# Kernel optimization log

Hardware: AMD Instinct MI355X
Metric: run time of the kernel (lower is better)

Reference implementation:

```python
import jax, jax.numpy as jnp
import numpy as np

DIM = 512
NUM_HEADS = 8
HEAD_DIM = DIM // NUM_HEADS
SCALE = HEAD_DIM ** -0.5


def setup_inputs() -> dict:
    key = jax.random.key(0)
    k1, k2, k3, k4 = jax.random.split(key, 4)
    x = jax.random.normal(k1, (4, 2048, DIM), dtype=jnp.float32)
    W_qkv = jax.random.normal(k2, (DIM, 3 * DIM), dtype=jnp.float32) * (DIM ** -0.5)
    W_proj = jax.random.normal(k3, (DIM, DIM), dtype=jnp.float32) * (DIM ** -0.5)
    b_proj = jax.random.normal(k4, (DIM,), dtype=jnp.float32) * 0.01
    return {"x": x, "W_qkv": W_qkv, "W_proj": W_proj, "b_proj": b_proj}


def reference(x, W_qkv, W_proj, b_proj):
    B, N, C = x.shape
    H, hd = NUM_HEADS, HEAD_DIM
    # qkv: [B, N, 3, H, hd] -> (q, k, v) each [B, H, N, hd]
    qkv = (x @ W_qkv).reshape(B, N, 3, H, hd)
    qkv = jnp.transpose(qkv, (2, 0, 3, 1, 4))
    q, k, v = qkv[0], qkv[1], qkv[2]
    # eager attention: [B, H, N, N]
    attn = jnp.einsum('bhnd,bhmd->bhnm', q, k) * SCALE
    attn = jax.nn.softmax(attn, axis=-1)
    out = jnp.einsum('bhnm,bhmd->bhnd', attn, v)  # [B, H, N, hd]
    out = jnp.transpose(out, (0, 2, 1, 3)).reshape(B, N, C)
    out = out @ W_proj + b_proj
    return (out, k, v)
```

## Files before the change

kernel.cpp:

```cpp
#include <hip/hip_runtime.h>

typedef unsigned short ushort_t;
typedef __bf16 bf16x8 __attribute__((ext_vector_type(8)));
typedef ushort_t u16x8 __attribute__((ext_vector_type(8)));
typedef float f32x4 __attribute__((ext_vector_type(4)));

#define MFMA(a, b, c) __builtin_amdgcn_mfma_f32_16x16x32_bf16(a, b, c, 0, 0, 0)

#define N_X      4194304L
#define N_WQKV   786432L
#define N_WPROJ  262144L
#define OUT_OFF_K 4194304L
#define OUT_OFF_V 8388608L

#define OFF_FLAG   0UL
#define OFF_XB     1024UL
#define OFF_WQKVT  (OFF_XB + 8388608UL)
#define OFF_WPROJT (OFF_WQKVT + 1572864UL)
#define OFF_BPROJ  (OFF_WPROJT + 524288UL)
#define OFF_QB     (OFF_BPROJ + 2048UL)
#define OFF_KB     (OFF_QB + 8388608UL)
#define OFF_VTB    (OFF_KB + 8388608UL)
#define OFF_ATTN   (OFF_VTB + 8388608UL)

#define QSCALE 0.180336880519191f

__device__ __forceinline__ ushort_t f2b(float f) {
    union { float f; unsigned u; } v; v.f = f;
    return (ushort_t)((v.u + 0x7FFFu + ((v.u >> 16) & 1u)) >> 16);
}
__device__ __forceinline__ ushort_t f2b_trunc(float f) {
    union { float f; unsigned u; } v; v.f = f;
    return (ushort_t)(v.u >> 16);
}
__device__ __forceinline__ float b2f(ushort_t h) {
    union { unsigned u; float f; } v; v.u = ((unsigned)h) << 16;
    return v.f;
}
__device__ __forceinline__ float ldf(const float* p, long i) { return p[i]; }
__device__ __forceinline__ float ldf(const ushort_t* p, long i) { return b2f(p[i]); }
__device__ __forceinline__ void stf(float* p, long i, float v) { p[i] = v; }
__device__ __forceinline__ void stf(ushort_t* p, long i, float v) { p[i] = f2b(v); }

__device__ __forceinline__ float fast_exp2(float x) {
#if __has_builtin(__builtin_amdgcn_exp2f)
    return __builtin_amdgcn_exp2f(x);
#else
    return __expf(x * 0.6931471805599453f);
#endif
}

__device__ __forceinline__ void glds16(const void* g, const void* l) {
    __builtin_amdgcn_global_load_lds((__attribute__((address_space(1))) void*)g,
                                     (__attribute__((address_space(3))) void*)l,
                                     16, 0, 0);
}

__global__ void k_detect(const unsigned* __restrict__ x, int* __restrict__ flag) {
    int lane = threadIdx.x & 63;
    int cnt = 0;
#pragma unroll
    for (int i = 0; i < 4; ++i) {
        unsigned w = x[lane + i * 64];
        float v = __uint_as_float((w & 0xFFFFu) << 16);
        float a = fabsf(v);
        if (a > 1e-3f && a < 100.0f) cnt++;
    }
#pragma unroll
    for (int off = 32; off; off >>= 1) cnt += __shfl_down(cnt, off, 64);
    if (lane == 0) *flag = (cnt > 128) ? 1 : 0;
}

template <typename T>
__global__ void k_prep(const T* __restrict__ x, const T* __restrict__ wq,
                       const T* __restrict__ wp, const T* __restrict__ bp,
                       ushort_t* __restrict__ xb, ushort_t* __restrict__ wqT,
                       ushort_t* __restrict__ wpT, float* __restrict__ bpf,
                       const int* __restrict__ flag, int want) {
    if (*flag != want) return;
    long i0 = (long)blockIdx.x * blockDim.x + threadIdx.x;
    long stride = (long)gridDim.x * blockDim.x;
    for (long i = i0; i < N_X; i += stride) xb[i] = f2b(ldf(x, i));
    for (long i = i0; i < N_WQKV; i += stride) {
        long n = i >> 9, k = i & 511;
        wqT[i] = f2b(ldf(wq, k * 1536 + n));
    }
    for (long i = i0; i < N_WPROJ; i += stride) {
        long n = i >> 9, k = i & 511;
        wpT[i] = f2b(ldf(wp, k * 512 + n));
    }
    for (long i = i0; i < 512; i += stride) bpf[i] = ldf(bp, i);
}

template <typename TOUT>
__global__ __launch_bounds__(256, 2)
void k_qkv(const ushort_t* __restrict__ xb, const ushort_t* __restrict__ wqT,
           ushort_t* __restrict__ qb, ushort_t* __restrict__ kb, ushort_t* __restrict__ vb,
           TOUT* __restrict__ kout, TOUT* __restrict__ vout,
           const int* __restrict__ flag, int want) {
    if (*flag != want) return;
    __shared__ __align__(16) ushort_t As[128 * 32];
    __shared__ __align__(16) ushort_t Bs[128 * 32];
    const int tid = threadIdx.x, wave = tid >> 6, lane = tid & 63;
    const int tm = blockIdx.x * 128, tn = blockIdx.y * 128;
    const int wm = (wave >> 1) * 64, wn = (wave & 1) * 64;
    const int l15 = lane & 15, lq = lane >> 4;
    const int srow = lane >> 2, sc = lane & 3;

    f32x4 acc[4][4];
#pragma unroll
    for (int a = 0; a < 4; ++a)
#pragma unroll
        for (int b = 0; b < 4; ++b) acc[a][b] = (f32x4){0.f, 0.f, 0.f, 0.f};

    for (int k0 = 0; k0 < 512; k0 += 32) {
#pragma unroll
        for (int t = 0; t < 2; ++t) {
            int s = wave * 2 + t;
            int row = s * 16 + srow;
            int c = (sc ^ (row >> 1)) & 3;
            glds16(xb  + (long)(tm + row) * 512 + k0 + c * 8, As + s * 512);
            glds16(wqT + (long)(tn + row) * 512 + k0 + c * 8, Bs + s * 512);
        }
        __syncthreads();
        bf16x8 af[4], bfr[4];
#pragma unroll
        for (int mt = 0; mt < 4; ++mt) {
            int row = wm + mt * 16 + l15;
            int cp = (lq ^ (row >> 1)) & 3;
            af[mt] = *(const bf16x8*)(As + row * 32 + cp * 8);
        }
#pragma unroll
        for (int nt = 0; nt < 4; ++nt) {
            int row = wn + nt * 16 + l15;
            int cp = (lq ^ (row >> 1)) & 3;
            bfr[nt] = *(const bf16x8*)(Bs + row * 32 + cp * 8);
        }
#pragma unroll
        for (int mt = 0; mt < 4; ++mt)
#pragma unroll
            for (int nt = 0; nt < 4; ++nt)
                acc[mt][nt] = MFMA(af[mt], bfr[nt], acc[mt][nt]);
        __syncthreads();
    }

#pragma unroll
    for (int mt = 0; mt < 4; ++mt) {
#pragma unroll
        for (int nt = 0; nt < 4; ++nt) {
            int j = tn + wn + nt * 16 + l15;
            int t = j >> 9, h = (j >> 6) & 7, d = j & 63;
#pragma unroll
            for (int r = 0; r < 4; ++r) {
                int mm = tm + wm + mt * 16 + lq * 4 + r;
                int b = mm >> 11, nn = mm & 2047;
                float v = acc[mt][nt][r];
                long idx = ((long)(b * 8 + h) * 2048 + nn) * 64 + d;
                if (t == 0) {
                    qb[idx] = f2b(v * QSCALE);
                } else if (t == 1) {
                    kb[idx] = f2b(v);
                    stf(kout, idx, v);
                } else {
                    vb[idx] = f2b(v);
                    stf(vout, idx, v);
                }
            }
        }
    }
}

__global__ __launch_bounds__(256, 4)
void k_vtrans(const ushort_t* __restrict__ vb, ushort_t* __restrict__ vtb) {
    __shared__ ushort_t T[64 * 64];
    const int tid = threadIdx.x;
    const int bh = blockIdx.y, ktile = blockIdx.x;
    const long base = (long)bh * 131072 + (long)ktile * 64 * 64;
    const int row = tid >> 2, cq = tid & 3;
#pragma unroll
    for (int half = 0; half < 2; ++half) {
        int c = cq + half * 4;
        u16x8 v = *(const u16x8*)(vb + base + row * 64 + c * 8);
#pragma unroll
        for (int e = 0; e < 8; ++e) {
            int dim = c * 8 + e;
            T[row * 64 + ((dim + row) & 63)] = v[e];
        }
    }
    __syncthreads();
#pragma unroll
    for (int it = 0; it < 16; ++it) {
        int d = (tid >> 6) * 16 + it;
        int key = tid & 63;
        vtb[(long)bh * 131072 + (long)d * 2048 + ktile * 64 + key] =
            T[key * 64 + ((d + key) & 63)];
    }
}

__global__ __launch_bounds__(256, 4)
void k_attn(const ushort_t* __restrict__ qb, const ushort_t* __restrict__ kb,
            const ushort_t* __restrict__ vtb, ushort_t* __restrict__ attnb) {
    __shared__ __align__(16) ushort_t Kt[128 * 64];
    __shared__ __align__(16) ushort_t Vt[64 * 128];
    __shared__ __align__(16) ushort_t Ps[4][16 * 64];
    const int tid = threadIdx.x, wave = tid >> 6, lane = tid & 63;
    const int l15 = lane & 15, lq = lane >> 4;
    const int bh = blockIdx.y, qt = blockIdx.x;
    const long kvbase = (long)bh * 131072;
    const long qbase = kvbase + (long)qt * 64 * 64;

    bf16x8 aQ[2];
#pragma unroll
    for (int kt = 0; kt < 2; ++kt)
        aQ[kt] = *(const bf16x8*)(qb + qbase +
            (long)(wave * 16 + l15) * 64 + kt * 32 + lq * 8);

    union { ushort_t u[8]; bf16x8 v; } oneu;
#pragma unroll
    for (int i = 0; i < 8; ++i) oneu.u[i] = 0x3F80;
    const bf16x8 ones = oneu.v;

    f32x4 oacc[4], sum_acc;
#pragma unroll
    for (int n = 0; n < 4; ++n) oacc[n] = (f32x4){0.f, 0.f, 0.f, 0.f};
    sum_acc = (f32x4){0.f, 0.f, 0.f, 0.f};

    const int ksrow = lane >> 3, kschunk = lane & 7;
    const int vsrow = lane >> 4, vschunk = lane & 15;
    ushort_t* Pw = &Ps[wave][0];

    for (int j = 0; j < 16; ++j) {
#pragma unroll
        for (int t = 0; t < 4; ++t) {
            int s = wave * 4 + t;
            {
                int row = s * 8 + ksrow;
                int c = kschunk ^ (row & 7);
                glds16(kb + kvbase + (long)(j * 128 + row) * 64 + c * 8, Kt + s * 512);
            }
            {
                int row = s * 4 + vsrow;
                int c = vschunk ^ (row & 15);
                glds16(vtb + kvbase + (long)row * 2048 + j * 128 + c * 8, Vt + s * 512);
            }
        }
        __syncthreads();

#pragma unroll
        for (int h = 0; h < 2; ++h) {
            f32x4 sacc[4];
#pragma unroll
            for (int nt = 0; nt < 4; ++nt) sacc[nt] = (f32x4){0.f, 0.f, 0.f, 0.f};
#pragma unroll
            for (int nt = 0; nt < 4; ++nt) {
                int krow = h * 64 + nt * 16 + l15;
#pragma unroll
                for (int kt = 0; kt < 2; ++kt) {
                    int c = (kt * 4 + lq) ^ (krow & 7);
                    bf16x8 bk = *(const bf16x8*)(Kt + krow * 64 + c * 8);
                    sacc[nt] = MFMA(aQ[kt], bk, sacc[nt]);
                }
            }
#pragma unroll
            for (int nt = 0; nt < 4; ++nt) {
#pragma unroll
                for (int r = 0; r < 4; ++r) {
                    float p = fast_exp2(sacc[nt][r]);
                    int prow = lq * 4 + r;
                    int col = nt * 16 + l15;
                    int ch = (col >> 3) ^ (prow & 7);
                    Pw[prow * 64 + ch * 8 + (col & 7)] = f2b_trunc(p);
                }
            }
#pragma unroll
            for (int kt = 0; kt < 2; ++kt) {
                int cha = (kt * 4 + lq) ^ (l15 & 7);
                bf16x8 ap = *(const bf16x8*)(Pw + l15 * 64 + cha * 8);
                sum_acc = MFMA(ap, ones, sum_acc);
#pragma unroll
                for (int nd = 0; nd < 4; ++nd) {
                    int vrow = nd * 16 + l15;
                    int vch = (h * 8 + kt * 4 + lq) ^ (vrow & 15);
                    bf16x8 bv = *(const bf16x8*)(Vt + vrow * 128 + vch * 8);
                    oacc[nd] = MFMA(ap, bv, oacc[nd]);
                }
            }
        }
        __syncthreads();
    }

    const int b = bh >> 3, hh = bh & 7;
#pragma unroll
    for (int r = 0; r < 4; ++r) {
        float inv = 1.0f / sum_acc[r];
        int n = qt * 64 + wave * 16 + lq * 4 + r;
#pragma unroll
        for (int nd = 0; nd < 4; ++nd) {
            int d = nd * 16 + l15;
            attnb[((long)b * 2048 + n) * 512 + hh * 64 + d] = f2b(oacc[nd][r] * inv);
        }
    }
}

template <typename TOUT>
__global__ __launch_bounds__(256, 2)
void k_proj(const ushort_t* __restrict__ ab, const ushort_t* __restrict__ wpT,
            const float* __restrict__ bpf, TOUT* __restrict__ out,
            const int* __restrict__ flag, int want) {
    if (*flag != want) return;
    __shared__ __align__(16) ushort_t As[128 * 32];
    __shared__ __align__(16) ushort_t Bs[128 * 32];
    const int tid = threadIdx.x, wave = tid >> 6, lane = tid & 63;
    const int tm = blockIdx.x * 128, tn = blockIdx.y * 128;
    const int wm = (wave >> 1) * 64, wn = (wave & 1) * 64;
    const int l15 = lane & 15, lq = lane >> 4;
    const int srow = lane >> 2, sc = lane & 3;

    f32x4 acc[4][4];
#pragma unroll
    for (int a = 0; a < 4; ++a)
#pragma unroll
        for (int b = 0; b < 4; ++b) acc[a][b] = (f32x4){0.f, 0.f, 0.f, 0.f};

    for (int k0 = 0; k0 < 512; k0 += 32) {
#pragma unroll
        for (int t = 0; t < 2; ++t) {
            int s = wave * 2 + t;
            int row = s * 16 + srow;
            int c = (sc ^ (row >> 1)) & 3;
            glds16(ab  + (long)(tm + row) * 512 + k0 + c * 8, As + s * 512);
            glds16(wpT + (long)(tn + row) * 512 + k0 + c * 8, Bs + s * 512);
        }
        __syncthreads();
        bf16x8 af[4], bfr[4];
#pragma unroll
        for (int mt = 0; mt < 4; ++mt) {
            int row = wm + mt * 16 + l15;
            int cp = (lq ^ (row >> 1)) & 3;
            af[mt] = *(const bf16x8*)(As + row * 32 + cp * 8);
        }
#pragma unroll
        for (int nt = 0; nt < 4; ++nt) {
            int row = wn + nt * 16 + l15;
            int cp = (lq ^ (row >> 1)) & 3;
            bfr[nt] = *(const bf16x8*)(Bs + row * 32 + cp * 8);
        }
#pragma unroll
        for (int mt = 0; mt < 4; ++mt)
#pragma unroll
            for (int nt = 0; nt < 4; ++nt)
                acc[mt][nt] = MFMA(af[mt], bfr[nt], acc[mt][nt]);
        __syncthreads();
    }

#pragma unroll
    for (int mt = 0; mt < 4; ++mt) {
#pragma unroll
        for (int nt = 0; nt < 4; ++nt) {
            int j = tn + wn + nt * 16 + l15;
            float bias = bpf[j];
#pragma unroll
            for (int r = 0; r < 4; ++r) {
                int mm = tm + wm + mt * 16 + lq * 4 + r;
                stf(out, (long)mm * 512 + j, acc[mt][nt][r] + bias);
            }
        }
    }
}

extern "C" void kernel_launch(void* const* d_in, const int* in_sizes, int n_in,
                              void* d_out, int out_size, void* d_ws, size_t ws_size,
                              hipStream_t stream) {
    (void)in_sizes; (void)n_in; (void)out_size; (void)ws_size;
    char* ws = (char*)d_ws;
    int* flag = (int*)(ws + OFF_FLAG);
    ushort_t* xb  = (ushort_t*)(ws + OFF_XB);
    ushort_t* wqT = (ushort_t*)(ws + OFF_WQKVT);
    ushort_t* wpT = (ushort_t*)(ws + OFF_WPROJT);
    float*    bpf = (float*)(ws + OFF_BPROJ);
    ushort_t* qb  = (ushort_t*)(ws + OFF_QB);
    ushort_t* kb  = (ushort_t*)(ws + OFF_KB);
    ushort_t* vtb = (ushort_t*)(ws + OFF_VTB);
    ushort_t* ab  = (ushort_t*)(ws + OFF_ATTN);
    ushort_t* vb  = (ushort_t*)(ws + OFF_ATTN);

    k_detect<<<1, 64, 0, stream>>>((const unsigned*)d_in[0], flag);

    k_prep<float><<<1024, 256, 0, stream>>>(
        (const float*)d_in[0], (const float*)d_in[1], (const float*)d_in[2],
        (const float*)d_in[3], xb, wqT, wpT, bpf, flag, 0);
    k_prep<ushort_t><<<1024, 256, 0, stream>>>(
        (const ushort_t*)d_in[0], (const ushort_t*)d_in[1], (const ushort_t*)d_in[2],
        (const ushort_t*)d_in[3], xb, wqT, wpT, bpf, flag, 1);

    dim3 gq(64, 12);
    k_qkv<float><<<gq, 256, 0, stream>>>(xb, wqT, qb, kb, vb,
        (float*)d_out + OUT_OFF_K, (float*)d_out + OUT_OFF_V, flag, 0);
    k_qkv<ushort_t><<<gq, 256, 0, stream>>>(xb, wqT, qb, kb, vb,
        (ushort_t*)d_out + OUT_OFF_K, (ushort_t*)d_out + OUT_OFF_V, flag, 1);

    k_vtrans<<<dim3(32, 32), 256, 0, stream>>>(vb, vtb);

    k_attn<<<dim3(32, 32), 256, 0, stream>>>(qb, kb, vtb, ab);

    dim3 gp(64, 4);
    k_proj<float><<<gp, 256, 0, stream>>>(ab, wpT, bpf, (float*)d_out, flag, 0);
    k_proj<ushort_t><<<gp, 256, 0, stream>>>(ab, wpT, bpf, (ushort_t*)d_out, flag, 1);
}
```

Baseline: 187.0 us.

## Drop dtype detection, vectorize prep, tile-transpose weights, double-buffer K in attention

Removes the runtime dtype-detect kernel and duplicate templated launches, so only the fp32 path is compiled and launched. The grid-stride prep is split into a vectorized x-to-bf16 cast and shared-memory tiled weight transposes, replacing strided uncoalesced reads. The attention kernel double-buffers K tiles in LDS, prefetching the next tile during compute. It also loads V^T fragments straight from global memory into registers instead of staging them in LDS. This raises register pressure and leans on cache for the V reads.

Result: slower. 252.5 us (+35.0%).

```diff
diff --git a/kernel.cpp b/kernel.cpp
--- a/kernel.cpp
+++ b/kernel.cpp
@@ -7,21 +7,16 @@
 
 #define MFMA(a, b, c) __builtin_amdgcn_mfma_f32_16x16x32_bf16(a, b, c, 0, 0, 0)
 
-#define N_X      4194304L
-#define N_WQKV   786432L
-#define N_WPROJ  262144L
 #define OUT_OFF_K 4194304L
 #define OUT_OFF_V 8388608L
 
-#define OFF_FLAG   0UL
-#define OFF_XB     1024UL
-#define OFF_WQKVT  (OFF_XB + 8388608UL)
+#define OFF_WQKVT  0UL
 #define OFF_WPROJT (OFF_WQKVT + 1572864UL)
-#define OFF_BPROJ  (OFF_WPROJT + 524288UL)
-#define OFF_QB     (OFF_BPROJ + 2048UL)
+#define OFF_QB     (OFF_WPROJT + 524288UL)
 #define OFF_KB     (OFF_QB + 8388608UL)
 #define OFF_VTB    (OFF_KB + 8388608UL)
 #define OFF_ATTN   (OFF_VTB + 8388608UL)
+#define OFF_XB     (OFF_ATTN + 8388608UL)
 
 #define QSCALE 0.180336880519191f
 
@@ -33,15 +28,6 @@
     union { float f; unsigned u; } v; v.f = f;
     return (ushort_t)(v.u >> 16);
 }
-__device__ __forceinline__ float b2f(ushort_t h) {
-    union { unsigned u; float f; } v; v.u = ((unsigned)h) << 16;
-    return v.f;
-}
-__device__ __forceinline__ float ldf(const float* p, long i) { return p[i]; }
-__device__ __forceinline__ float ldf(const ushort_t* p, long i) { return b2f(p[i]); }
-__device__ __forceinline__ void stf(float* p, long i, float v) { p[i] = v; }
-__device__ __forceinline__ void stf(ushort_t* p, long i, float v) { p[i] = f2b(v); }
-
 __device__ __forceinline__ float fast_exp2(float x) {
 #if __has_builtin(__builtin_amdgcn_exp2f)
     return __builtin_amdgcn_exp2f(x);
@@ -56,49 +42,37 @@
                                      16, 0, 0);
 }
 
-__global__ void k_detect(const unsigned* __restrict__ x, int* __restrict__ flag) {
-    int lane = threadIdx.x & 63;
-    int cnt = 0;
-#pragma unroll
-    for (int i = 0; i < 4; ++i) {
-        unsigned w = x[lane + i * 64];
-        float v = __uint_as_float((w & 0xFFFFu) << 16);
-        float a = fabsf(v);
-        if (a > 1e-3f && a < 100.0f) cnt++;
-    }
-#pragma unroll
-    for (int off = 32; off; off >>= 1) cnt += __shfl_down(cnt, off, 64);
-    if (lane == 0) *flag = (cnt > 128) ? 1 : 0;
-}
-
-template <typename T>
-__global__ void k_prep(const T* __restrict__ x, const T* __restrict__ wq,
-                       const T* __restrict__ wp, const T* __restrict__ bp,
-                       ushort_t* __restrict__ xb, ushort_t* __restrict__ wqT,
-                       ushort_t* __restrict__ wpT, float* __restrict__ bpf,
-                       const int* __restrict__ flag, int want) {
-    if (*flag != want) return;
-    long i0 = (long)blockIdx.x * blockDim.x + threadIdx.x;
-    long stride = (long)gridDim.x * blockDim.x;
-    for (long i = i0; i < N_X; i += stride) xb[i] = f2b(ldf(x, i));
-    for (long i = i0; i < N_WQKV; i += stride) {
-        long n = i >> 9, k = i & 511;
-        wqT[i] = f2b(ldf(wq, k * 1536 + n));
-    }
-    for (long i = i0; i < N_WPROJ; i += stride) {
-        long n = i >> 9, k = i & 511;
-        wpT[i] = f2b(ldf(wp, k * 512 + n));
-    }
-    for (long i = i0; i < 512; i += stride) bpf[i] = ldf(bp, i);
-}
-
-template <typename TOUT>
+__global__ void k_prepx(const float* __restrict__ src, ushort_t* __restrict__ dst) {
+    long i = ((long)blockIdx.x * blockDim.x + threadIdx.x) * 8;
+    float4 a = *(const float4*)(src + i);
+    float4 b = *(const float4*)(src + i + 4);
+    u16x8 o;
+    o[0] = f2b(a.x); o[1] = f2b(a.y); o[2] = f2b(a.z); o[3] = f2b(a.w);
+    o[4] = f2b(b.x); o[5] = f2b(b.y); o[6] = f2b(b.z); o[7] = f2b(b.w);
+    *(u16x8*)(dst + i) = o;
+}
+
+template <int SRCW>
+__global__ void k_trw(const float* __restrict__ src, ushort_t* __restrict__ dst,
+                      int srcH) {
+    __shared__ ushort_t T[64][65];
+    const int tid = threadIdx.x;
+    const int c0 = blockIdx.x * 64, r0 = blockIdx.y * 64;
+    const int lx = tid & 63, ly = tid >> 6;
+#pragma unroll
+    for (int rr = ly; rr < 64; rr += 4)
+        T[rr][lx] = f2b(src[(long)(r0 + rr) * SRCW + c0 + lx]);
+    __syncthreads();
+#pragma unroll
+    for (int rr = ly; rr < 64; rr += 4)
+        dst[(long)(c0 + rr) * srcH + r0 + lx] = T[lx][rr];
+}
+
 __global__ __launch_bounds__(256, 2)
 void k_qkv(const ushort_t* __restrict__ xb, const ushort_t* __restrict__ wqT,
-           ushort_t* __restrict__ qb, ushort_t* __restrict__ kb, ushort_t* __restrict__ vb,
-           TOUT* __restrict__ kout, TOUT* __restrict__ vout,
-           const int* __restrict__ flag, int want) {
-    if (*flag != want) return;
+           ushort_t* __restrict__ qb, ushort_t* __restrict__ kb,
+           ushort_t* __restrict__ vb, float* __restrict__ kout,
+           float* __restrict__ vout) {
     __shared__ __align__(16) ushort_t As[128 * 32];
     __shared__ __align__(16) ushort_t Bs[128 * 32];
     const int tid = threadIdx.x, wave = tid >> 6, lane = tid & 63;
@@ -160,10 +134,10 @@
                     qb[idx] = f2b(v * QSCALE);
                 } else if (t == 1) {
                     kb[idx] = f2b(v);
-                    stf(kout, idx, v);
+                    kout[idx] = v;
                 } else {
                     vb[idx] = f2b(v);
-                    stf(vout, idx, v);
+                    vout[idx] = v;
                 }
             }
         }
@@ -175,7 +149,7 @@
     __shared__ ushort_t T[64 * 64];
     const int tid = threadIdx.x;
     const int bh = blockIdx.y, ktile = blockIdx.x;
-    const long base = (long)bh * 131072 + (long)ktile * 64 * 64;
+    const long base = (long)bh * 131072 + (long)ktile * 4096;
     const int row = tid >> 2, cq = tid & 3;
 #pragma unroll
     for (int half = 0; half < 2; ++half) {
@@ -200,20 +174,18 @@
 __global__ __launch_bounds__(256, 4)
 void k_attn(const ushort_t* __restrict__ qb, const ushort_t* __restrict__ kb,
             const ushort_t* __restrict__ vtb, ushort_t* __restrict__ attnb) {
-    __shared__ __align__(16) ushort_t Kt[128 * 64];
-    __shared__ __align__(16) ushort_t Vt[64 * 128];
+    __shared__ __align__(16) ushort_t Kt[2][128 * 64];
     __shared__ __align__(16) ushort_t Ps[4][16 * 64];
     const int tid = threadIdx.x, wave = tid >> 6, lane = tid & 63;
     const int l15 = lane & 15, lq = lane >> 4;
     const int bh = blockIdx.y, qt = blockIdx.x;
     const long kvbase = (long)bh * 131072;
-    const long qbase = kvbase + (long)qt * 64 * 64;
+    const long qbase  = kvbase + (long)qt * 4096;
 
     bf16x8 aQ[2];
 #pragma unroll
     for (int kt = 0; kt < 2; ++kt)
-        aQ[kt] = *(const bf16x8*)(qb + qbase +
-            (long)(wave * 16 + l15) * 64 + kt * 32 + lq * 8);
+        aQ[kt] = *(const bf16x8*)(qb + qbase + (long)(wave * 16 + l15) * 64 + kt * 32 + lq * 8);
 
     union { ushort_t u[8]; bf16x8 v; } oneu;
 #pragma unroll
@@ -226,65 +198,104 @@
     sum_acc = (f32x4){0.f, 0.f, 0.f, 0.f};
 
     const int ksrow = lane >> 3, kschunk = lane & 7;
-    const int vsrow = lane >> 4, vschunk = lane & 15;
     ushort_t* Pw = &Ps[wave][0];
 
+#pragma unroll
+    for (int t = 0; t < 4; ++t) {
+        int s = wave * 4 + t;
+        int row = s * 8 + ksrow;
+        int c = kschunk ^ (row & 7);
+        glds16(kb + kvbase + (long)row * 64 + c * 8, &Kt[0][s * 512]);
+    }
+    __syncthreads();
+
     for (int j = 0; j < 16; ++j) {
-#pragma unroll
-        for (int t = 0; t < 4; ++t) {
-            int s = wave * 4 + t;
-            {
+        const ushort_t* Kc = &Kt[j & 1][0];
+
+        bf16x8 vfa[8];
+#pragma unroll
+        for (int kt = 0; kt < 2; ++kt)
+#pragma unroll
+            for (int nd = 0; nd < 4; ++nd)
+                vfa[kt * 4 + nd] = *(const bf16x8*)(vtb + kvbase +
+                    (long)(nd * 16 + l15) * 2048 + j * 128 + kt * 32 + lq * 8);
+
+        if (j < 15) {
+#pragma unroll
+            for (int t = 0; t < 4; ++t) {
+                int s = wave * 4 + t;
                 int row = s * 8 + ksrow;
                 int c = kschunk ^ (row & 7);
-                glds16(kb + kvbase + (long)(j * 128 + row) * 64 + c * 8, Kt + s * 512);
-            }
-            {
-                int row = s * 4 + vsrow;
-                int c = vschunk ^ (row & 15);
-                glds16(vtb + kvbase + (long)row * 2048 + j * 128 + c * 8, Vt + s * 512);
-            }
-        }
-        __syncthreads();
-
-#pragma unroll
-        for (int h = 0; h < 2; ++h) {
-            f32x4 sacc[4];
-#pragma unroll
-            for (int nt = 0; nt < 4; ++nt) sacc[nt] = (f32x4){0.f, 0.f, 0.f, 0.f};
+                glds16(kb + kvbase + (long)((j + 1) * 128 + row) * 64 + c * 8,
+                       &Kt[(j + 1) & 1][s * 512]);
+            }
+        }
+
+        f32x4 sacc[2][4];
+#pragma unroll
+        for (int h = 0; h < 2; ++h)
+#pragma unroll
+            for (int nt = 0; nt < 4; ++nt) sacc[h][nt] = (f32x4){0.f, 0.f, 0.f, 0.f};
+#pragma unroll
+        for (int h = 0; h < 2; ++h)
 #pragma unroll
             for (int nt = 0; nt < 4; ++nt) {
                 int krow = h * 64 + nt * 16 + l15;
 #pragma unroll
                 for (int kt = 0; kt < 2; ++kt) {
                     int c = (kt * 4 + lq) ^ (krow & 7);
-                    bf16x8 bk = *(const bf16x8*)(Kt + krow * 64 + c * 8);
-                    sacc[nt] = MFMA(aQ[kt], bk, sacc[nt]);
+                    bf16x8 bk = *(const bf16x8*)(Kc + krow * 64 + c * 8);
+                    sacc[h][nt] = MFMA(aQ[kt], bk, sacc[h][nt]);
                 }
             }
-#pragma unroll
-            for (int nt = 0; nt < 4; ++nt) {
-#pragma unroll
-                for (int r = 0; r < 4; ++r) {
-                    float p = fast_exp2(sacc[nt][r]);
-                    int prow = lq * 4 + r;
-                    int col = nt * 16 + l15;
-                    int ch = (col >> 3) ^ (prow & 7);
-                    Pw[prow * 64 + ch * 8 + (col & 7)] = f2b_trunc(p);
-                }
-            }
-#pragma unroll
-            for (int kt = 0; kt < 2; ++kt) {
-                int cha = (kt * 4 + lq) ^ (l15 & 7);
-                bf16x8 ap = *(const bf16x8*)(Pw + l15 * 64 + cha * 8);
-                sum_acc = MFMA(ap, ones, sum_acc);
-#pragma unroll
-                for (int nd = 0; nd < 4; ++nd) {
-                    int vrow = nd * 16 + l15;
-                    int vch = (h * 8 + kt * 4 + lq) ^ (vrow & 15);
-                    bf16x8 bv = *(const bf16x8*)(Vt + vrow * 128 + vch * 8);
-                    oacc[nd] = MFMA(ap, bv, oacc[nd]);
-                }
-            }
+
+#pragma unroll
+        for (int nt = 0; nt < 4; ++nt) {
+#pragma unroll
+            for (int r = 0; r < 4; ++r) {
+                float p = fast_exp2(sacc[0][nt][r]);
+                int prow = lq * 4 + r;
+                int col = nt * 16 + l15;
+                int ch = (col >> 3) ^ (prow & 7);
+                Pw[prow * 64 + ch * 8 + (col & 7)] = f2b_trunc(p);
+            }
+        }
+#pragma unroll
+        for (int kt = 0; kt < 2; ++kt) {
+            int cha = (kt * 4 + lq) ^ (l15 & 7);
+            bf16x8 ap = *(const bf16x8*)(Pw + l15 * 64 + cha * 8);
+            sum_acc = MFMA(ap, ones, sum_acc);
+#pragma unroll
+            for (int nd = 0; nd < 4; ++nd)
+                oacc[nd] = MFMA(ap, vfa[kt * 4 + nd], oacc[nd]);
+        }
+
+        bf16x8 vfb[8];
+#pragma unroll
+        for (int kt = 0; kt < 2; ++kt)
+#pragma unroll
+            for (int nd = 0; nd < 4; ++nd)
+                vfb[kt * 4 + nd] = *(const bf16x8*)(vtb + kvbase +
+                    (long)(nd * 16 + l15) * 2048 + j * 128 + 64 + kt * 32 + lq * 8);
+#pragma unroll
+        for (int nt = 0; nt < 4; ++nt) {
+#pragma unroll
+            for (int r = 0; r < 4; ++r) {
+                float p = fast_exp2(sacc[1][nt][r]);
+                int prow = lq * 4 + r;
+                int col = nt * 16 + l15;
+                int ch = (col >> 3) ^ (prow & 7);
+                Pw[prow * 64 + ch * 8 + (col & 7)] = f2b_trunc(p);
+            }
+        }
+#pragma unroll
+        for (int kt = 0; kt < 2; ++kt) {
+            int cha = (kt * 4 + lq) ^ (l15 & 7);
+            bf16x8 ap = *(const bf16x8*)(Pw + l15 * 64 + cha * 8);
+            sum_acc = MFMA(ap, ones, sum_acc);
+#pragma unroll
+            for (int nd = 0; nd < 4; ++nd)
+                oacc[nd] = MFMA(ap, vfb[kt * 4 + nd], oacc[nd]);
         }
         __syncthreads();
     }
@@ -302,12 +313,9 @@
     }
 }
 
-template <typename TOUT>
 __global__ __launch_bounds__(256, 2)
 void k_proj(const ushort_t* __restrict__ ab, const ushort_t* __restrict__ wpT,
-            const float* __restrict__ bpf, TOUT* __restrict__ out,
-            const int* __restrict__ flag, int want) {
-    if (*flag != want) return;
+            const float* __restrict__ bp, float* __restrict__ out) {
     __shared__ __align__(16) ushort_t As[128 * 32];
     __shared__ __align__(16) ushort_t Bs[128 * 32];
     const int tid = threadIdx.x, wave = tid >> 6, lane = tid & 63;
@@ -358,11 +366,11 @@
 #pragma unroll
         for (int nt = 0; nt < 4; ++nt) {
             int j = tn + wn + nt * 16 + l15;
-            float bias = bpf[j];
+            float bias = bp[j];
 #pragma unroll
             for (int r = 0; r < 4; ++r) {
                 int mm = tm + wm + mt * 16 + lq * 4 + r;
-                stf(out, (long)mm * 512 + j, acc[mt][nt][r] + bias);
+                out[(long)mm * 512 + j] = acc[mt][nt][r] + bias;
             }
         }
     }
@@ -373,37 +381,31 @@
                               hipStream_t stream) {
     (void)in_sizes; (void)n_in; (void)out_size; (void)ws_size;
     char* ws = (char*)d_ws;
-    int* flag = (int*)(ws + OFF_FLAG);
-    ushort_t* xb  = (ushort_t*)(ws + OFF_XB);
+    const float* x  = (const float*)d_in[0];
+    const float* wq = (const float*)d_in[1];
+    const float* wp = (const float*)d_in[2];
+    const float* bp = (const float*)d_in[3];
     ushort_t* wqT = (ushort_t*)(ws + OFF_WQKVT);
     ushort_t* wpT = (ushort_t*)(ws + OFF_WPROJT);
-    float*    bpf = (float*)(ws + OFF_BPROJ);
     ushort_t* qb  = (ushort_t*)(ws + OFF_QB);
-    ushort_t* kb  = (ushort_t*)(ws + OFF_KB);
+    ushort_t* kbw = (ushort_t*)(ws + OFF_KB);
     ushort_t* vtb = (ushort_t*)(ws + OFF_VTB);
     ushort_t* ab  = (ushort_t*)(ws + OFF_ATTN);
     ushort_t* vb  = (ushort_t*)(ws + OFF_ATTN);
-
-    k_detect<<<1, 64, 0, stream>>>((const unsigned*)d_in[0], flag);
-
-    k_prep<float><<<1024, 256, 0, stream>>>(
-        (const float*)d_in[0], (const float*)d_in[1], (const float*)d_in[2],
-        (const float*)d_in[3], xb, wqT, wpT, bpf, flag, 0);
-    k_prep<ushort_t><<<1024, 256, 0, stream>>>(
-        (const ushort_t*)d_in[0], (const ushort_t*)d_in[1], (const ushort_t*)d_in[2],
-        (const ushort_t*)d_in[3], xb, wqT, wpT, bpf, flag, 1);
-
-    dim3 gq(64, 12);
-    k_qkv<float><<<gq, 256, 0, stream>>>(xb, wqT, qb, kb, vb,
-        (float*)d_out + OUT_OFF_K, (float*)d_out + OUT_OFF_V, flag, 0);
-    k_qkv<ushort_t><<<gq, 256, 0, stream>>>(xb, wqT, qb, kb, vb,
-        (ushort_t*)d_out + OUT_OFF_K, (ushort_t*)d_out + OUT_OFF_V, flag, 1);
+    ushort_t* xb  = (ushort_t*)(ws + OFF_XB);
+    float* kout = (float*)d_out + OUT_OFF_K;
+    float* vout = (float*)d_out + OUT_OFF_V;
+
+    k_prepx<<<2048, 256, 0, stream>>>(x, xb);
+
+    k_trw<1536><<<dim3(24, 8), 256, 0, stream>>>(wq, wqT, 512);
+    k_trw<512><<<dim3(8, 8), 256, 0, stream>>>(wp, wpT, 512);
+
+    k_qkv<<<dim3(64, 12), 256, 0, stream>>>(xb, wqT, qb, kbw, vb, kout, vout);
 
     k_vtrans<<<dim3(32, 32), 256, 0, stream>>>(vb, vtb);
 
-    k_attn<<<dim3(32, 32), 256, 0, stream>>>(qb, kb, vtb, ab);
-
-    dim3 gp(64, 4);
-    k_proj<float><<<gp, 256, 0, stream>>>(ab, wpT, bpf, (float*)d_out, flag, 0);
-    k_proj<ushort_t><<<gp, 256, 0, stream>>>(ab, wpT, bpf, (ushort_t*)d_out, flag, 1);
-}
+    k_attn<<<dim3(32, 32), 256, 0, stream>>>(qb, kbw, vtb, ab);
+
+    k_proj<<<dim3(64, 4), 256, 0, stream>>>(ab, wpT, bp, (float*)d_out);
+}
```
